# Performance work log

Measured on AMD Instinct MI355X. Metric: run time of the kernel, lower is better.

Reference implementation:

```python
import jax, jax.numpy as jnp
import numpy as np

N = 20000       # nodes
C = 64          # channels per irrep
E = 320000      # edges (avg degree 16)
S = 64          # num_species
R = 8           # radial embedding dim
HR = 64         # radial MLP hidden
HEADS = 2       # readout heads
AVG = 16.0      # avg_num_neighbors
SOFT = 2.0      # soft_normalization


def setup_inputs() -> dict:
    key = jax.random.key(0)
    ks = jax.random.split(key, 28)
    g = lambda k, sh, sc=1.0: jax.random.normal(k, sh, dtype=jnp.float32) * sc
    inv = lambda n: 1.0 / float(np.sqrt(n))
    return {
        "edge_vectors": g(ks[0], (E, 3)),
        "node_feats_s": g(ks[1], (N, C)),
        "node_feats_v": g(ks[2], (N, C, 3)),
        "radial_embeddings": g(ks[3], (E, R)),
        "node_species": jax.random.randint(ks[4], (N,), 0, S),
        "senders": jax.random.randint(ks[5], (E,), 0, N),
        "receivers": jax.random.randint(ks[6], (E,), 0, N),
        # residual FullyConnectedTensorProduct(feats, one-hot species) weights
        "W_rs": g(ks[7], (S, C, C), inv(C)),
        "W_rv": g(ks[8], (S, C, C), inv(C)),
        # interaction: linear up, radial MLP (5 TP paths), linear down
        "W_up_s": g(ks[9], (C, C), inv(C)),
        "W_up_v": g(ks[10], (C, C), inv(C)),
        "Wr1": g(ks[11], (R, HR), inv(R)),
        "Wr2": g(ks[12], (HR, 5 * C), inv(HR)),
        "W_down_s": g(ks[13], (C, C), inv(C)),
        "W_down_v": g(ks[14], (C, C), inv(C)),
        # equivariant product basis: per-channel species-indexed symmetric-contraction weights
        "w1s": g(ks[15], (S, C)),
        "w1v": g(ks[16], (S, C)),
        "w2ss": g(ks[17], (S, C)),
        "w2vv": g(ks[18], (S, C)),
        "w2sv": g(ks[19], (S, C)),
        "W_prod_s": g(ks[20], (C, C), inv(C)),
        "W_prod_v": g(ks[21], (C, C), inv(C)),
        # linear readout heads (out_irreps -> 1x0e per head)
        "w_read": g(ks[22], (HEADS, C), inv(C)),
    }


def reference(edge_vectors, node_feats_s, node_feats_v, radial_embeddings,
              node_species, senders, receivers,
              W_rs, W_rv, W_up_s, W_up_v, Wr1, Wr2, W_down_s, W_down_v,
              w1s, w1v, w2ss, w2vv, w2sv, W_prod_s, W_prod_v, w_read):
    n_nodes = node_feats_s.shape[0]
    sp = node_species

    # --- residual connection: FCTP(feats, one-hot(species)) == species-indexed channel mix
    res_s = jnp.einsum('nc,ncd->nd', node_feats_s, W_rs[sp])
    res_v = jnp.einsum('ncx,ncd->ndx', node_feats_v, W_rv[sp])

    # --- InteractionBlock ---
    s_u = node_feats_s @ W_up_s
    v_u = jnp.einsum('ncx,cd->ndx', node_feats_v, W_up_v)
    nrm = jnp.linalg.norm(edge_vectors, axis=-1, keepdims=True)
    u = edge_vectors / jnp.maximum(nrm, 1e-9)  # l=1 spherical harmonic direction [E,3]
    # radial MLP -> per-edge per-channel weights for the 5 CG paths of (0e+1o)x(0e+1o)->0e+1o
    w = (jax.nn.silu(radial_embeddings @ Wr1) @ Wr2).reshape(-1, 5, s_u.shape[1])
    se = s_u[senders]            # [E,C] gather (irregular)
    ve = v_u[senders]            # [E,C,3]
    dot = jnp.einsum('ecx,ex->ec', ve, u)          # 1o x 1o -> 0e
    crs = jnp.cross(ve, u[:, None, :])             # 1o x 1o -> 1o
    m_s = w[:, 0] * se + w[:, 3] * dot
    m_v = (w[:, 1][..., None] * ve
           + w[:, 2][..., None] * u[:, None, :]
           + w[:, 4][..., None] * crs)
    a_s = jax.ops.segment_sum(m_s, receivers, num_segments=n_nodes) / AVG
    a_v = jax.ops.segment_sum(m_v, receivers, num_segments=n_nodes) / AVG
    a_s = a_s @ W_down_s
    a_v = jnp.einsum('ncx,cd->ndx', a_v, W_down_v)

    # --- EquivariantProductBasisBlock: symmetric contraction (correlation<=2), per-channel
    # species-indexed weights, followed by a linear to out_irreps ---
    vv = jnp.sum(a_v * a_v, axis=-1)                                   # 1o (x) 1o -> 0e
    p_s = w1s[sp] * a_s + w2ss[sp] * a_s * a_s + w2vv[sp] * vv
    p_v = w1v[sp][..., None] * a_v + w2sv[sp][..., None] * a_s[..., None] * a_v
    p_s = p_s @ W_prod_s
    p_v = jnp.einsum('ncx,cd->ndx', p_v, W_prod_v)

    # --- soft normalization: phi(n) = 1/(1 + n*sus(n)), n = norm/SOFT ---
    def sus(x):
        return jnp.where(x > 0, jnp.exp(-1.0 / jnp.where(x > 0, x, 1.0)), 0.0)

    def phi(n):
        n = n / SOFT
        return 1.0 / (1.0 + n * sus(n))

    f_s = p_s * phi(jnp.abs(p_s))
    f_v = p_v * phi(jnp.linalg.norm(p_v, axis=-1, keepdims=True))

    # --- residual add ---
    f_s = f_s + res_s
    f_v = f_v + res_v

    # --- readout heads (Linear out_irreps -> 1x0e), stacked on axis=1 ---
    node_out = jnp.einsum('nc,hc->nh', f_s, w_read)
    return (node_out, f_s, f_v)
```

## Files before the change

kernel.cpp:

```cpp
#include <hip/hip_runtime.h>

#define N_NODES 20000
#define C 64
#define E_EDGES 320000
#define S_SPEC 64
#define R_DIM 8
#define HR 64
#define HEADS 2
#define TE 64
#define NT (E_EDGES/TE)
#define HPAD 68
#define INV_AVG (1.0f/16.0f)

#define FS_OFF 40000
#define FV_OFF 1320000

typedef short bf16x4 __attribute__((ext_vector_type(4)));
typedef float f32x4  __attribute__((ext_vector_type(4)));

__device__ __forceinline__ unsigned short f2bf(float f){
  unsigned u = __float_as_uint(f);
  u += 0x7fffu + ((u >> 16) & 1u);
  return (unsigned short)(u >> 16);
}
__device__ __forceinline__ float bf2f(unsigned short b){
  return __uint_as_float(((unsigned)b) << 16);
}
__device__ __forceinline__ float phi_f(float x){
  float n = x * 0.5f;
  float s = (n > 0.0f) ? expf(-1.0f/n) : 0.0f;
  return 1.0f / (1.0f + n * s);
}

__global__ __launch_bounds__(256) void wr2t_kernel(const float* __restrict__ Wr2,
                                                   unsigned short* __restrict__ wr2t){
  int idx = blockIdx.x*256 + threadIdx.x;
  int n = idx >> 6, k = idx & 63;
  wr2t[idx] = f2bf(Wr2[k*320 + n] * INV_AVG);
}

__global__ __launch_bounds__(256) void node_up_kernel(
    const float* __restrict__ fs, const float* __restrict__ fv,
    const float* __restrict__ Wus, const float* __restrict__ Wuv,
    ushort4* __restrict__ suv){
  const int ni = threadIdx.x >> 6;
  const int d  = threadIdx.x & 63;
  const int n  = blockIdx.x*4 + ni;
  __shared__ float s_l[4][C];
  __shared__ float v_l[4][3][C];
  s_l[ni][d] = fs[n*C + d];
  #pragma unroll
  for (int x = 0; x < 3; ++x) v_l[ni][x][d] = fv[(n*C + d)*3 + x];
  __syncthreads();
  float as = 0.f, a0 = 0.f, a1 = 0.f, a2 = 0.f;
  #pragma unroll 4
  for (int c = 0; c < C; ++c){
    float wsv = Wus[c*C + d];
    float wvv = Wuv[c*C + d];
    as += s_l[ni][c] * wsv;
    a0 += v_l[ni][0][c] * wvv;
    a1 += v_l[ni][1][c] * wvv;
    a2 += v_l[ni][2][c] * wvv;
  }
  ushort4 o;
  o.x = f2bf(as); o.y = f2bf(a0); o.z = f2bf(a1); o.w = f2bf(a2);
  suv[(size_t)n*C + d] = o;
}

__global__ __launch_bounds__(256) void hist_kernel(const int* __restrict__ rcv, int* __restrict__ count){
  int e = blockIdx.x*256 + threadIdx.x;
  atomicAdd(&count[rcv[e]], 1);
}

__global__ __launch_bounds__(1024) void scan_kernel(const int* __restrict__ count, int* __restrict__ cursor){
  __shared__ int sums[1024];
  const int t = threadIdx.x;
  const int base = t*20;
  int s = 0;
  #pragma unroll 4
  for (int i = 0; i < 20; ++i){ int idx = base+i; if (idx < N_NODES) s += count[idx]; }
  sums[t] = s;
  __syncthreads();
  for (int off = 1; off < 1024; off <<= 1){
    int v = (t >= off) ? sums[t-off] : 0;
    __syncthreads();
    sums[t] += v;
    __syncthreads();
  }
  int run = (t > 0) ? sums[t-1] : 0;
  for (int i = 0; i < 20; ++i){
    int idx = base+i;
    if (idx < N_NODES){ cursor[idx] = run; run += count[idx]; }
  }
}

__global__ __launch_bounds__(256) void scatter_kernel(
    const int* __restrict__ snd, const int* __restrict__ rcv,
    const float* __restrict__ ev, const float* __restrict__ re,
    int* __restrict__ cursor,
    int* __restrict__ snd_s, int* __restrict__ rcv_s,
    float4* __restrict__ u_s, float* __restrict__ re_s){
  int e = blockIdx.x*256 + threadIdx.x;
  int r = rcv[e];
  int pos = atomicAdd(&cursor[r], 1);
  snd_s[pos] = snd[e];
  rcv_s[pos] = r;
  float x = ev[e*3+0], y = ev[e*3+1], z = ev[e*3+2];
  float nr = sqrtf(x*x + y*y + z*z);
  float inv = 1.0f / fmaxf(nr, 1e-9f);
  float4 u4; u4.x = x*inv; u4.y = y*inv; u4.z = z*inv; u4.w = 0.f;
  u_s[pos] = u4;
  const float4* rp = (const float4*)&re[(size_t)e*R_DIM];
  float4 ra = rp[0], rb = rp[1];
  float4* op = (float4*)&re_s[(size_t)pos*R_DIM];
  op[0] = ra; op[1] = rb;
}

__global__ __launch_bounds__(512, 6) void edge_kernel(
    const float4* __restrict__ u_s, const float* __restrict__ re_s,
    const int* __restrict__ snd_s, const int* __restrict__ rcv_s,
    const float* __restrict__ Wr1, const unsigned short* __restrict__ wr2t,
    const ushort4* __restrict__ suv,
    float* __restrict__ a_s, float* __restrict__ a_v)
{
  __shared__ __align__(16) float Wr1_l[R_DIM*HR];
  __shared__ __align__(16) unsigned short Wr2T_l[320*HPAD];

  const int t = threadIdx.x;
  const int lane = t & 63;
  const int w = t >> 6;
  const int g  = w >> 1;
  const int h2 = w & 1;
  int b = blockIdx.x;
  int xcd = b & 7, idx = b >> 3;
  const int tile = xcd * (NT >> 3) + idx;
  const int e0 = tile * TE;

  Wr1_l[t] = Wr1[t];
  #pragma unroll
  for (int j = 0; j < 10; ++j){
    int i4 = t + 512*j;
    ushort4 v4 = ((const ushort4*)wr2t)[i4];
    int el = i4*4; int n = el >> 6, k = el & 63;
    *(ushort4*)&Wr2T_l[n*HPAD + k] = v4;
  }

  const int arow = g*16 + (lane & 15);
  const int koff = 4*(lane >> 4);
  const int cl = lane & 15;
  const int ebase = g*16 + (lane >> 4)*4;
  float4 ra = ((const float4*)&re_s[(size_t)(e0 + arow)*R_DIM])[0];
  float4 rb = ((const float4*)&re_s[(size_t)(e0 + arow)*R_DIM])[1];
  float u4x[4], u4y[4], u4z[4];
  int sn4[4], rc4[4];
  #pragma unroll
  for (int i = 0; i < 4; ++i){
    int e = e0 + ebase + i;
    float4 uu = u_s[e];
    u4x[i] = uu.x; u4y[i] = uu.y; u4z[i] = uu.z;
    sn4[i] = snd_s[e];
    rc4[i] = rcv_s[e];
  }
  __syncthreads();

  bf16x4 ha[4];
  #pragma unroll
  for (int kt = 0; kt < 4; ++kt){
    short4 tmp;
    #pragma unroll
    for (int j = 0; j < 4; ++j){
      int k = kt*16 + koff + j;
      float acc = ra.x*Wr1_l[0*HR+k] + ra.y*Wr1_l[1*HR+k] + ra.z*Wr1_l[2*HR+k] + ra.w*Wr1_l[3*HR+k]
                + rb.x*Wr1_l[4*HR+k] + rb.y*Wr1_l[5*HR+k] + rb.z*Wr1_l[6*HR+k] + rb.w*Wr1_l[7*HR+k];
      float sil = acc / (1.0f + expf(-acc));
      ((unsigned short*)&tmp)[j] = f2bf(sil);
    }
    ha[kt] = *(bf16x4*)&tmp;
  }

  ushort4 gv[4][2];
  #pragma unroll
  for (int i = 0; i < 4; ++i){
    const ushort4* sp_ = &suv[(size_t)sn4[i]*C];
    #pragma unroll
    for (int kk = 0; kk < 2; ++kk) gv[i][kk] = sp_[(2*h2 + kk)*16 + cl];
  }

  f32x4 acc[10];
  #pragma unroll
  for (int lf = 0; lf < 10; ++lf) acc[lf] = (f32x4){0.f,0.f,0.f,0.f};
  #pragma unroll
  for (int kt = 0; kt < 4; ++kt){
    bf16x4 af = ha[kt];
    #pragma unroll
    for (int lf = 0; lf < 10; ++lf){
      int p = lf >> 1, kk = lf & 1;
      int n = (p*4 + 2*h2 + kk)*16 + cl;
      bf16x4 bf = *(const bf16x4*)&Wr2T_l[n*HPAD + kt*16 + koff];
      acc[lf] = __builtin_amdgcn_mfma_f32_16x16x16bf16_1k(af, bf, acc[lf], 0, 0, 0);
    }
  }

  {
    float ms[2], mv0[2], mv1[2], mv2[2];
    #pragma unroll
    for (int kk = 0; kk < 2; ++kk){ ms[kk]=0.f; mv0[kk]=0.f; mv1[kk]=0.f; mv2[kk]=0.f; }
    int cur = rc4[0];
    #pragma unroll
    for (int i = 0; i < 4; ++i){
      int rc = rc4[i];
      if (rc != cur){
        #pragma unroll
        for (int kk = 0; kk < 2; ++kk){
          int c = (2*h2 + kk)*16 + cl;
          unsafeAtomicAdd(&a_s[cur*C + c],       ms[kk]);
          unsafeAtomicAdd(&a_v[(cur*3+0)*C + c], mv0[kk]);
          unsafeAtomicAdd(&a_v[(cur*3+1)*C + c], mv1[kk]);
          unsafeAtomicAdd(&a_v[(cur*3+2)*C + c], mv2[kk]);
          ms[kk]=0.f; mv0[kk]=0.f; mv1[kk]=0.f; mv2[kk]=0.f;
        }
        cur = rc;
      }
      float u0 = u4x[i], u1 = u4y[i], u2 = u4z[i];
      #pragma unroll
      for (int kk = 0; kk < 2; ++kk){
        float se  = bf2f(gv[i][kk].x);
        float ve0 = bf2f(gv[i][kk].y);
        float ve1 = bf2f(gv[i][kk].z);
        float ve2 = bf2f(gv[i][kk].w);
        float w0 = acc[0*2+kk][i];
        float w1 = acc[1*2+kk][i];
        float w2 = acc[2*2+kk][i];
        float w3 = acc[3*2+kk][i];
        float w4 = acc[4*2+kk][i];
        float dt  = ve0*u0 + ve1*u1 + ve2*u2;
        float cr0 = ve1*u2 - ve2*u1;
        float cr1 = ve2*u0 - ve0*u2;
        float cr2 = ve0*u1 - ve1*u0;
        ms[kk]  += w0*se + w3*dt;
        mv0[kk] += w1*ve0 + w2*u0 + w4*cr0;
        mv1[kk] += w1*ve1 + w2*u1 + w4*cr1;
        mv2[kk] += w1*ve2 + w2*u2 + w4*cr2;
      }
    }
    #pragma unroll
    for (int kk = 0; kk < 2; ++kk){
      int c = (2*h2 + kk)*16 + cl;
      unsafeAtomicAdd(&a_s[cur*C + c],       ms[kk]);
      unsafeAtomicAdd(&a_v[(cur*3+0)*C + c], mv0[kk]);
      unsafeAtomicAdd(&a_v[(cur*3+1)*C + c], mv1[kk]);
      unsafeAtomicAdd(&a_v[(cur*3+2)*C + c], mv2[kk]);
    }
  }
}

__global__ __launch_bounds__(256) void node_post_kernel(
    const float* __restrict__ a_s, const float* __restrict__ a_v,
    const float* __restrict__ fs_in, const float* __restrict__ fv_in,
    const int* __restrict__ species,
    const float* __restrict__ W_rs, const float* __restrict__ W_rv,
    const float* __restrict__ W_ds, const float* __restrict__ W_dv,
    const float* __restrict__ w1s, const float* __restrict__ w1v,
    const float* __restrict__ w2ss, const float* __restrict__ w2vv, const float* __restrict__ w2sv,
    const float* __restrict__ W_ps, const float* __restrict__ W_pv,
    const float* __restrict__ w_read, float* __restrict__ out)
{
  const int ni = threadIdx.x >> 6;
  const int d  = threadIdx.x & 63;
  const int n  = blockIdx.x*4 + ni;
  const int sp = species[n];
  __shared__ float as_l[4][C];
  __shared__ float av_l[4][3][C];
  __shared__ float si_l[4][C];
  __shared__ float vi_l[4][3][C];
  as_l[ni][d] = a_s[n*C + d];
  #pragma unroll
  for (int x=0;x<3;x++) av_l[ni][x][d] = a_v[(n*3+x)*C + d];
  si_l[ni][d] = fs_in[n*C + d];
  #pragma unroll
  for (int x=0;x<3;x++) vi_l[ni][x][d] = fv_in[(n*C + d)*3 + x];
  __syncthreads();
  const float* Wrs_p = W_rs + sp*C*C;
  const float* Wrv_p = W_rv + sp*C*C;
  float bs=0, bv0=0, bv1=0, bv2=0, rs=0, rv0=0, rv1=0, rv2=0;
  for (int c=0;c<C;++c){
    float wds = W_ds[c*C+d], wdv = W_dv[c*C+d];
    float wrs = Wrs_p[c*C+d], wrv = Wrv_p[c*C+d];
    bs  += as_l[ni][c]*wds;
    bv0 += av_l[ni][0][c]*wdv; bv1 += av_l[ni][1][c]*wdv; bv2 += av_l[ni][2][c]*wdv;
    rs  += si_l[ni][c]*wrs;
    rv0 += vi_l[ni][0][c]*wrv; rv1 += vi_l[ni][1][c]*wrv; rv2 += vi_l[ni][2][c]*wrv;
  }
  float vv = bv0*bv0 + bv1*bv1 + bv2*bv2;
  float ps  = w1s[sp*C+d]*bs + w2ss[sp*C+d]*bs*bs + w2vv[sp*C+d]*vv;
  float c1v = w1v[sp*C+d], c2sv = w2sv[sp*C+d];
  float pv0 = c1v*bv0 + c2sv*bs*bv0;
  float pv1 = c1v*bv1 + c2sv*bs*bv1;
  float pv2 = c1v*bv2 + c2sv*bs*bv2;
  __syncthreads();
  as_l[ni][d] = ps; av_l[ni][0][d]=pv0; av_l[ni][1][d]=pv1; av_l[ni][2][d]=pv2;
  __syncthreads();
  float qs=0, qv0=0, qv1=0, qv2=0;
  for (int c=0;c<C;++c){
    float wps = W_ps[c*C+d], wpv = W_pv[c*C+d];
    qs  += as_l[ni][c]*wps;
    qv0 += av_l[ni][0][c]*wpv; qv1 += av_l[ni][1][c]*wpv; qv2 += av_l[ni][2][c]*wpv;
  }
  float fsv = qs * phi_f(fabsf(qs)) + rs;
  float nv = sqrtf(qv0*qv0 + qv1*qv1 + qv2*qv2);
  float ph = phi_f(nv);
  float fv0 = qv0*ph + rv0;
  float fv1 = qv1*ph + rv1;
  float fv2 = qv2*ph + rv2;
  out[FS_OFF + n*C + d] = fsv;
  float* fvo = &out[FV_OFF + (size_t)(n*C + d)*3];
  fvo[0]=fv0; fvo[1]=fv1; fvo[2]=fv2;
  #pragma unroll
  for (int h=0; h<HEADS; ++h){
    float r = fsv * w_read[h*C + d];
    #pragma unroll
    for (int off=32; off>0; off>>=1) r += __shfl_down(r, off);
    if (d == 0) out[n*HEADS + h] = r;
  }
}

extern "C" void kernel_launch(void* const* d_in, const int* in_sizes, int n_in,
                              void* d_out, int out_size, void* d_ws, size_t ws_size,
                              hipStream_t stream)
{
  const float* ev   = (const float*)d_in[0];
  const float* nfs  = (const float*)d_in[1];
  const float* nfv  = (const float*)d_in[2];
  const float* re   = (const float*)d_in[3];
  const int*   spec = (const int*)d_in[4];
  const int*   snd  = (const int*)d_in[5];
  const int*   rcv  = (const int*)d_in[6];
  const float* W_rs = (const float*)d_in[7];
  const float* W_rv = (const float*)d_in[8];
  const float* Wus  = (const float*)d_in[9];
  const float* Wuv  = (const float*)d_in[10];
  const float* Wr1  = (const float*)d_in[11];
  const float* Wr2  = (const float*)d_in[12];
  const float* Wds  = (const float*)d_in[13];
  const float* Wdv  = (const float*)d_in[14];
  const float* w1s  = (const float*)d_in[15];
  const float* w1v  = (const float*)d_in[16];
  const float* w2ss = (const float*)d_in[17];
  const float* w2vv = (const float*)d_in[18];
  const float* w2sv = (const float*)d_in[19];
  const float* Wps  = (const float*)d_in[20];
  const float* Wpv  = (const float*)d_in[21];
  const float* wrd  = (const float*)d_in[22];

  float* out = (float*)d_out;
  float* ws  = (float*)d_ws;
  ushort4* suv  = (ushort4*)ws;
  float*   a_s  = ws + 2560000;
  float*   a_v  = ws + 3840000;
  int*    count = (int*)(ws + 7680000);
  int*    cursr = (int*)(ws + 7700000);
  int*    snd_s = (int*)(ws + 7720000);
  int*    rcv_s = (int*)(ws + 8040000);
  float4* u_s   = (float4*)(ws + 8360000);
  float*  re_s  = ws + 9640000;
  unsigned short* wr2t = (unsigned short*)(ws + 12200000);

  hipMemsetAsync(a_s, 0, (size_t)5120000*sizeof(float), stream);
  hipMemsetAsync(count, 0, (size_t)N_NODES*sizeof(int), stream);

  wr2t_kernel<<<(320*64)/256, 256, 0, stream>>>(Wr2, wr2t);
  node_up_kernel<<<N_NODES/4, 256, 0, stream>>>(nfs, nfv, Wus, Wuv, suv);
  hist_kernel<<<E_EDGES/256, 256, 0, stream>>>(rcv, count);
  scan_kernel<<<1, 1024, 0, stream>>>(count, cursr);
  scatter_kernel<<<E_EDGES/256, 256, 0, stream>>>(snd, rcv, ev, re, cursr,
                                                  snd_s, rcv_s, u_s, re_s);
  edge_kernel<<<NT, 512, 0, stream>>>(u_s, re_s, snd_s, rcv_s, Wr1, wr2t,
                                      suv, a_s, a_v);
  node_post_kernel<<<N_NODES/4, 256, 0, stream>>>(a_s, a_v, nfs, nfv, spec,
      W_rs, W_rv, Wds, Wdv, w1s, w1v, w2ss, w2vv, w2sv, Wps, Wpv, wrd, out);
}
```

Before: 409.1 us.

## Move node GEMMs to bf16 MFMA and group residual GEMM by species

The per-node scalar dot-product kernels are replaced by 64-node tiles computed with bf16 16x16x16 MFMA instructions. This covers the up-projection, the down-projection and the product linear. The species-indexed residual tensor product is split into its own GEMM kernel over a species-sorted node permutation, built by new histogram, scan and permute kernels. Each block then loads one species' weight matrix once, instead of every node fetching its own 64x64 slice. The residual is stored as bf16 in the workspace that the up-projection used, which adds bf16 rounding to residual and post-node results and adds several small launches.

```diff
diff --git a/kernel.cpp b/kernel.cpp
--- a/kernel.cpp
+++ b/kernel.cpp
@@ -11,6 +11,8 @@
 #define NT (E_EDGES/TE)
 #define HPAD 68
 #define INV_AVG (1.0f/16.0f)
+#define NB 64
+#define NNB ((N_NODES + NB - 1)/NB)
 
 #define FS_OFF 40000
 #define FV_OFF 1320000
@@ -39,32 +41,78 @@
   wr2t[idx] = f2bf(Wr2[k*320 + n] * INV_AVG);
 }
 
-__global__ __launch_bounds__(256) void node_up_kernel(
+__global__ __launch_bounds__(256) void node_up_mfma(
     const float* __restrict__ fs, const float* __restrict__ fv,
     const float* __restrict__ Wus, const float* __restrict__ Wuv,
     ushort4* __restrict__ suv){
-  const int ni = threadIdx.x >> 6;
-  const int d  = threadIdx.x & 63;
-  const int n  = blockIdx.x*4 + ni;
-  __shared__ float s_l[4][C];
-  __shared__ float v_l[4][3][C];
-  s_l[ni][d] = fs[n*C + d];
-  #pragma unroll
-  for (int x = 0; x < 3; ++x) v_l[ni][x][d] = fv[(n*C + d)*3 + x];
+  __shared__ __align__(16) unsigned short A[4][NB][HPAD];
+  __shared__ __align__(16) unsigned short B[2][NB][HPAD];
+  const int t = threadIdx.x;
+  const int n0 = blockIdx.x * NB;
+  #pragma unroll
+  for (int j = 0; j < 4; ++j){
+    int el = (t + 256*j)*4; int row = el >> 6, c = el & 63;
+    float4 v = (n0+row < N_NODES) ? *(const float4*)&fs[(size_t)(n0+row)*C + c]
+                                  : (float4){0,0,0,0};
+    ushort4 o; o.x=f2bf(v.x); o.y=f2bf(v.y); o.z=f2bf(v.z); o.w=f2bf(v.w);
+    *(ushort4*)&A[0][row][c] = o;
+  }
+  #pragma unroll
+  for (int j = 0; j < 16; ++j){
+    int el = t + 256*j; int row = el >> 6, c = el & 63;
+    float x=0,y=0,z=0;
+    if (n0+row < N_NODES){
+      const float* p = &fv[((size_t)(n0+row)*C + c)*3];
+      x = p[0]; y = p[1]; z = p[2];
+    }
+    A[1][row][c] = f2bf(x); A[2][row][c] = f2bf(y); A[3][row][c] = f2bf(z);
+  }
+  #pragma unroll
+  for (int j = 0; j < 16; ++j){
+    int el = t + 256*j; int c = el >> 6, d = el & 63;
+    B[0][d][c] = f2bf(Wus[c*C + d]);
+    B[1][d][c] = f2bf(Wuv[c*C + d]);
+  }
   __syncthreads();
-  float as = 0.f, a0 = 0.f, a1 = 0.f, a2 = 0.f;
-  #pragma unroll 4
-  for (int c = 0; c < C; ++c){
-    float wsv = Wus[c*C + d];
-    float wvv = Wuv[c*C + d];
-    as += s_l[ni][c] * wsv;
-    a0 += v_l[ni][0][c] * wvv;
-    a1 += v_l[ni][1][c] * wvv;
-    a2 += v_l[ni][2][c] * wvv;
-  }
-  ushort4 o;
-  o.x = f2bf(as); o.y = f2bf(a0); o.z = f2bf(a1); o.w = f2bf(a2);
-  suv[(size_t)n*C + d] = o;
+  const int lane = t & 63, w = t >> 6;
+  const int arow = w*16 + (lane & 15);
+  const int koff = 4*(lane >> 4);
+  f32x4 acc[4][4];
+  #pragma unroll
+  for (int a=0;a<4;a++)
+    #pragma unroll
+    for (int cf=0;cf<4;cf++) acc[a][cf] = (f32x4){0,0,0,0};
+  #pragma unroll
+  for (int kt = 0; kt < 4; ++kt){
+    bf16x4 a0 = *(const bf16x4*)&A[0][arow][kt*16+koff];
+    bf16x4 a1 = *(const bf16x4*)&A[1][arow][kt*16+koff];
+    bf16x4 a2 = *(const bf16x4*)&A[2][arow][kt*16+koff];
+    bf16x4 a3 = *(const bf16x4*)&A[3][arow][kt*16+koff];
+    #pragma unroll
+    for (int cf = 0; cf < 4; ++cf){
+      const int brow = cf*16 + (lane & 15);
+      bf16x4 b0 = *(const bf16x4*)&B[0][brow][kt*16+koff];
+      bf16x4 b1 = *(const bf16x4*)&B[1][brow][kt*16+koff];
+      acc[0][cf] = __builtin_amdgcn_mfma_f32_16x16x16bf16_1k(a0, b0, acc[0][cf], 0,0,0);
+      acc[1][cf] = __builtin_amdgcn_mfma_f32_16x16x16bf16_1k(a1, b1, acc[1][cf], 0,0,0);
+      acc[2][cf] = __builtin_amdgcn_mfma_f32_16x16x16bf16_1k(a2, b1, acc[2][cf], 0,0,0);
+      acc[3][cf] = __builtin_amdgcn_mfma_f32_16x16x16bf16_1k(a3, b1, acc[3][cf], 0,0,0);
+    }
+  }
+  #pragma unroll
+  for (int i = 0; i < 4; ++i){
+    int n = n0 + w*16 + (lane>>4)*4 + i;
+    if (n < N_NODES){
+      #pragma unroll
+      for (int cf = 0; cf < 4; ++cf){
+        int c = cf*16 + (lane & 15);
+        ushort4 o;
+        o.x = f2bf(acc[0][cf][i]); o.y = f2bf(acc[1][cf][i]);
+        o.z = f2bf(acc[2][cf][i]); o.w = f2bf(acc[3][cf][i]);
+        suv[(size_t)n*C + c] = o;
+      }
+    }
+  }
 }
 
 __global__ __launch_bounds__(256) void hist_kernel(const int* __restrict__ rcv, int* __restrict__ count){
@@ -114,6 +162,109 @@
   float4 ra = rp[0], rb = rp[1];
   float4* op = (float4*)&re_s[(size_t)pos*R_DIM];
   op[0] = ra; op[1] = rb;
+}
+
+__global__ __launch_bounds__(256) void sp_hist_kernel(const int* __restrict__ sp, int* __restrict__ spcount){
+  int n = blockIdx.x*256 + threadIdx.x;
+  if (n < N_NODES) atomicAdd(&spcount[sp[n]], 1);
+}
+__global__ __launch_bounds__(64) void sp_scan_kernel(const int* __restrict__ spcount,
+                                                     int* __restrict__ spoff, int* __restrict__ spcur){
+  if (threadIdx.x == 0){
+    int run = 0;
+    for (int i = 0; i < S_SPEC; ++i){ spoff[i] = run; spcur[i] = run; run += spcount[i]; }
+    spoff[S_SPEC] = run;
+  }
+}
+__global__ __launch_bounds__(256) void sp_perm_kernel(const int* __restrict__ sp,
+                                                      int* __restrict__ spcur, int* __restrict__ perm_sp){
+  int n = blockIdx.x*256 + threadIdx.x;
+  if (n < N_NODES){
+    int pos = atomicAdd(&spcur[sp[n]], 1);
+    perm_sp[pos] = n;
+  }
+}
+
+__global__ __launch_bounds__(256) void residual_gemm(
+    const float* __restrict__ nfs, const float* __restrict__ nfv,
+    const float* __restrict__ W_rs, const float* __restrict__ W_rv,
+    const int* __restrict__ spoff, const int* __restrict__ perm_sp,
+    ushort4* __restrict__ resp){
+  const int s = blockIdx.x >> 3;
+  const int chunk = blockIdx.x & 7;
+  const int base = spoff[s];
+  const int cnt  = spoff[s+1] - base;
+  const int r0 = chunk * NB;
+  if (r0 >= cnt) return;
+  const int rows = min(NB, cnt - r0);
+  __shared__ __align__(16) unsigned short A[4][NB][HPAD];
+  __shared__ __align__(16) unsigned short B[2][NB][HPAD];
+  __shared__ int nid[NB];
+  const int t = threadIdx.x;
+  if (t < NB) nid[t] = (t < rows) ? perm_sp[base + r0 + t] : -1;
+  __syncthreads();
+  #pragma unroll
+  for (int j = 0; j < 16; ++j){
+    int el = t + 256*j; int row = el >> 6, c = el & 63;
+    int n = nid[row];
+    float sv=0, x=0, y=0, z=0;
+    if (n >= 0){
+      sv = nfs[(size_t)n*C + c];
+      const float* p = &nfv[((size_t)n*C + c)*3];
+      x = p[0]; y = p[1]; z = p[2];
+    }
+    A[0][row][c] = f2bf(sv); A[1][row][c] = f2bf(x);
+    A[2][row][c] = f2bf(y);  A[3][row][c] = f2bf(z);
+  }
+  const float* Ws = W_rs + (size_t)s*C*C;
+  const float* Wv = W_rv + (size_t)s*C*C;
+  #pragma unroll
+  for (int j = 0; j < 16; ++j){
+    int el = t + 256*j; int c = el >> 6, d = el & 63;
+    B[0][d][c] = f2bf(Ws[c*C + d]);
+    B[1][d][c] = f2bf(Wv[c*C + d]);
+  }
+  __syncthreads();
+  const int lane = t & 63, w = t >> 6;
+  const int arow = w*16 + (lane & 15);
+  const int koff = 4*(lane >> 4);
+  f32x4 acc[4][4];
+  #pragma unroll
+  for (int a=0;a<4;a++)
+    #pragma unroll
+    for (int cf=0;cf<4;cf++) acc[a][cf] = (f32x4){0,0,0,0};
+  #pragma unroll
+  for (int kt = 0; kt < 4; ++kt){
+    bf16x4 a0 = *(const bf16x4*)&A[0][arow][kt*16+koff];
+    bf16x4 a1 = *(const bf16x4*)&A[1][arow][kt*16+koff];
+    bf16x4 a2 = *(const bf16x4*)&A[2][arow][kt*16+koff];
+    bf16x4 a3 = *(const bf16x4*)&A[3][arow][kt*16+koff];
+    #pragma unroll
+    for (int cf = 0; cf < 4; ++cf){
+      const int brow = cf*16 + (lane & 15);
+      bf16x4 b0 = *(const bf16x4*)&B[0][brow][kt*16+koff];
+      bf16x4 b1 = *(const bf16x4*)&B[1][brow][kt*16+koff];
+      acc[0][cf] = __builtin_amdgcn_mfma_f32_16x16x16bf16_1k(a0, b0, acc[0][cf], 0,0,0);
+      acc[1][cf] = __builtin_amdgcn_mfma_f32_16x16x16bf16_1k(a1, b1, acc[1][cf], 0,0,0);
+      acc[2][cf] = __builtin_amdgcn_mfma_f32_16x16x16bf16_1k(a2, b1, acc[2][cf], 0,0,0);
+      acc[3][cf] = __builtin_amdgcn_mfma_f32_16x16x16bf16_1k(a3, b1, acc[3][cf], 0,0,0);
+    }
+  }
+  #pragma unroll
+  for (int i = 0; i < 4; ++i){
+    int row = w*16 + (lane>>4)*4 + i;
+    int n = nid[row];
+    if (n >= 0){
+      #pragma unroll
+      for (int cf = 0; cf < 4; ++cf){
+        int c = cf*16 + (lane & 15);
+        ushort4 o;
+        o.x = f2bf(acc[0][cf][i]); o.y = f2bf(acc[1][cf][i]);
+        o.z = f2bf(acc[2][cf][i]); o.w = f2bf(acc[3][cf][i]);
+        resp[(size_t)n*C + c] = o;
+      }
+    }
+  }
 }
 
 __global__ __launch_bounds__(512, 6) void edge_kernel(
@@ -254,73 +405,158 @@
   }
 }
 
-__global__ __launch_bounds__(256) void node_post_kernel(
+__global__ __launch_bounds__(256) void node_post_mfma(
     const float* __restrict__ a_s, const float* __restrict__ a_v,
-    const float* __restrict__ fs_in, const float* __restrict__ fv_in,
     const int* __restrict__ species,
-    const float* __restrict__ W_rs, const float* __restrict__ W_rv,
     const float* __restrict__ W_ds, const float* __restrict__ W_dv,
     const float* __restrict__ w1s, const float* __restrict__ w1v,
     const float* __restrict__ w2ss, const float* __restrict__ w2vv, const float* __restrict__ w2sv,
     const float* __restrict__ W_ps, const float* __restrict__ W_pv,
+    const ushort4* __restrict__ resp,
     const float* __restrict__ w_read, float* __restrict__ out)
 {
-  const int ni = threadIdx.x >> 6;
-  const int d  = threadIdx.x & 63;
-  const int n  = blockIdx.x*4 + ni;
-  const int sp = species[n];
-  __shared__ float as_l[4][C];
-  __shared__ float av_l[4][3][C];
-  __shared__ float si_l[4][C];
-  __shared__ float vi_l[4][3][C];
-  as_l[ni][d] = a_s[n*C + d];
-  #pragma unroll
-  for (int x=0;x<3;x++) av_l[ni][x][d] = a_v[(n*3+x)*C + d];
-  si_l[ni][d] = fs_in[n*C + d];
-  #pragma unroll
-  for (int x=0;x<3;x++) vi_l[ni][x][d] = fv_in[(n*C + d)*3 + x];
+  __shared__ __align__(16) unsigned short A[4][NB][HPAD];
+  __shared__ __align__(16) unsigned short B[4][NB][HPAD];
+  __shared__ int spl[NB];
+  const int t = threadIdx.x;
+  const int n0 = blockIdx.x * NB;
+  #pragma unroll
+  for (int j = 0; j < 4; ++j){
+    int el = (t + 256*j)*4; int row = el >> 6, c = el & 63;
+    bool ok = (n0+row < N_NODES);
+    float4 v0 = ok ? *(const float4*)&a_s[(size_t)(n0+row)*C + c] : (float4){0,0,0,0};
+    ushort4 o0; o0.x=f2bf(v0.x); o0.y=f2bf(v0.y); o0.z=f2bf(v0.z); o0.w=f2bf(v0.w);
+    *(ushort4*)&A[0][row][c] = o0;
+    #pragma unroll
+    for (int x = 0; x < 3; ++x){
+      float4 v = ok ? *(const float4*)&a_v[((size_t)(n0+row)*3 + x)*C + c] : (float4){0,0,0,0};
+      ushort4 o; o.x=f2bf(v.x); o.y=f2bf(v.y); o.z=f2bf(v.z); o.w=f2bf(v.w);
+      *(ushort4*)&A[1+x][row][c] = o;
+    }
+  }
+  #pragma unroll
+  for (int j = 0; j < 16; ++j){
+    int el = t + 256*j; int c = el >> 6, d = el & 63;
+    B[0][d][c] = f2bf(W_ds[c*C + d]);
+    B[1][d][c] = f2bf(W_dv[c*C + d]);
+    B[2][d][c] = f2bf(W_ps[c*C + d]);
+    B[3][d][c] = f2bf(W_pv[c*C + d]);
+  }
+  if (t < NB) spl[t] = (n0 + t < N_NODES) ? species[n0 + t] : 0;
   __syncthreads();
-  const float* Wrs_p = W_rs + sp*C*C;
-  const float* Wrv_p = W_rv + sp*C*C;
-  float bs=0, bv0=0, bv1=0, bv2=0, rs=0, rv0=0, rv1=0, rv2=0;
-  for (int c=0;c<C;++c){
-    float wds = W_ds[c*C+d], wdv = W_dv[c*C+d];
-    float wrs = Wrs_p[c*C+d], wrv = Wrv_p[c*C+d];
-    bs  += as_l[ni][c]*wds;
-    bv0 += av_l[ni][0][c]*wdv; bv1 += av_l[ni][1][c]*wdv; bv2 += av_l[ni][2][c]*wdv;
-    rs  += si_l[ni][c]*wrs;
-    rv0 += vi_l[ni][0][c]*wrv; rv1 += vi_l[ni][1][c]*wrv; rv2 += vi_l[ni][2][c]*wrv;
-  }
-  float vv = bv0*bv0 + bv1*bv1 + bv2*bv2;
-  float ps  = w1s[sp*C+d]*bs + w2ss[sp*C+d]*bs*bs + w2vv[sp*C+d]*vv;
-  float c1v = w1v[sp*C+d], c2sv = w2sv[sp*C+d];
-  float pv0 = c1v*bv0 + c2sv*bs*bv0;
-  float pv1 = c1v*bv1 + c2sv*bs*bv1;
-  float pv2 = c1v*bv2 + c2sv*bs*bv2;
+
+  const int lane = t & 63, w = t >> 6;
+  const int arow = w*16 + (lane & 15);
+  const int koff = 4*(lane >> 4);
+  const int cl = lane & 15;
+
+  f32x4 acc1[4][4];
+  #pragma unroll
+  for (int a=0;a<4;a++)
+    #pragma unroll
+    for (int cf=0;cf<4;cf++) acc1[a][cf] = (f32x4){0,0,0,0};
+  #pragma unroll
+  for (int kt = 0; kt < 4; ++kt){
+    bf16x4 a0 = *(const bf16x4*)&A[0][arow][kt*16+koff];
+    bf16x4 a1 = *(const bf16x4*)&A[1][arow][kt*16+koff];
+    bf16x4 a2 = *(const bf16x4*)&A[2][arow][kt*16+koff];
+    bf16x4 a3 = *(const bf16x4*)&A[3][arow][kt*16+koff];
+    #pragma unroll
+    for (int cf = 0; cf < 4; ++cf){
+      const int brow = cf*16 + (lane & 15);
+      bf16x4 b0 = *(const bf16x4*)&B[0][brow][kt*16+koff];
+      bf16x4 b1 = *(const bf16x4*)&B[1][brow][kt*16+koff];
+      acc1[0][cf] = __builtin_amdgcn_mfma_f32_16x16x16bf16_1k(a0, b0, acc1[0][cf], 0,0,0);
+      acc1[1][cf] = __builtin_amdgcn_mfma_f32_16x16x16bf16_1k(a1, b1, acc1[1][cf], 0,0,0);
+      acc1[2][cf] = __builtin_amdgcn_mfma_f32_16x16x16bf16_1k(a2, b1, acc1[2][cf], 0,0,0);
+      acc1[3][cf] = __builtin_amdgcn_mfma_f32_16x16x16bf16_1k(a3, b1, acc1[3][cf], 0,0,0);
+    }
+  }
+  #pragma unroll
+  for (int i = 0; i < 4; ++i){
+    int row = w*16 + (lane>>4)*4 + i;
+    int sp = spl[row];
+    #pragma unroll
+    for (int cf = 0; cf < 4; ++cf){
+      int c = cf*16 + cl;
+      float bs = acc1[0][cf][i], bv0 = acc1[1][cf][i], bv1 = acc1[2][cf][i], bv2 = acc1[3][cf][i];
+      float vv = bv0*bv0 + bv1*bv1 + bv2*bv2;
+      float ps = w1s[sp*C+c]*bs + w2ss[sp*C+c]*bs*bs + w2vv[sp*C+c]*vv;
+      float c1v = w1v[sp*C+c], c2sv = w2sv[sp*C+c];
+      A[0][row][c] = f2bf(ps);
+      A[1][row][c] = f2bf(c1v*bv0 + c2sv*bs*bv0);
+      A[2][row][c] = f2bf(c1v*bv1 + c2sv*bs*bv1);
+      A[3][row][c] = f2bf(c1v*bv2 + c2sv*bs*bv2);
+    }
+  }
   __syncthreads();
-  as_l[ni][d] = ps; av_l[ni][0][d]=pv0; av_l[ni][1][d]=pv1; av_l[ni][2][d]=pv2;
-  __syncthreads();
-  float qs=0, qv0=0, qv1=0, qv2=0;
-  for (int c=0;c<C;++c){
-    float wps = W_ps[c*C+d], wpv = W_pv[c*C+d];
-    qs  += as_l[ni][c]*wps;
-    qv0 += av_l[ni][0][c]*wpv; qv1 += av_l[ni][1][c]*wpv; qv2 += av_l[ni][2][c]*wpv;
-  }
-  float fsv = qs * phi_f(fabsf(qs)) + rs;
-  float nv = sqrtf(qv0*qv0 + qv1*qv1 + qv2*qv2);
-  float ph = phi_f(nv);
-  float fv0 = qv0*ph + rv0;
-  float fv1 = qv1*ph + rv1;
-  float fv2 = qv2*ph + rv2;
-  out[FS_OFF + n*C + d] = fsv;
-  float* fvo = &out[FV_OFF + (size_t)(n*C + d)*3];
-  fvo[0]=fv0; fvo[1]=fv1; fvo[2]=fv2;
-  #pragma unroll
-  for (int h=0; h<HEADS; ++h){
-    float r = fsv * w_read[h*C + d];
-    #pragma unroll
-    for (int off=32; off>0; off>>=1) r += __shfl_down(r, off);
-    if (d == 0) out[n*HEADS + h] = r;
+  f32x4 acc2[4][4];
+  #pragma unroll
+  for (int a=0;a<4;a++)
+    #pragma unroll
+    for (int cf=0;cf<4;cf++) acc2[a][cf] = (f32x4){0,0,0,0};
+  #pragma unroll
+  for (int kt = 0; kt < 4; ++kt){
+    bf16x4 a0 = *(const bf16x4*)&A[0][arow][kt*16+koff];
+    bf16x4 a1 = *(const bf16x4*)&A[1][arow][kt*16+koff];
+    bf16x4 a2 = *(const bf16x4*)&A[2][arow][kt*16+koff];
+    bf16x4 a3 = *(const bf16x4*)&A[3][arow][kt*16+koff];
+    #pragma unroll
+    for (int cf = 0; cf < 4; ++cf){
+      const int brow = cf*16 + (lane & 15);
+      bf16x4 b2 = *(const bf16x4*)&B[2][brow][kt*16+koff];
+      bf16x4 b3 = *(const bf16x4*)&B[3][brow][kt*16+koff];
+      acc2[0][cf] = __builtin_amdgcn_mfma_f32_16x16x16bf16_1k(a0, b2, acc2[0][cf], 0,0,0);
+      acc2[1][cf] = __builtin_amdgcn_mfma_f32_16x16x16bf16_1k(a1, b3, acc2[1][cf], 0,0,0);
+      acc2[2][cf] = __builtin_amdgcn_mfma_f32_16x16x16bf16_1k(a2, b3, acc2[2][cf], 0,0,0);
+      acc2[3][cf] = __builtin_amdgcn_mfma_f32_16x16x16bf16_1k(a3, b3, acc2[3][cf], 0,0,0);
+    }
+  }
+  float fsv_r[4][4];
+  #pragma unroll
+  for (int i = 0; i < 4; ++i){
+    int row = w*16 + (lane>>4)*4 + i;
+    int n = n0 + row;
+    bool ok = (n < N_NODES);
+    #pragma unroll
+    for (int cf = 0; cf < 4; ++cf){
+      int c = cf*16 + cl;
+      float qs = acc2[0][cf][i], qv0 = acc2[1][cf][i], qv1 = acc2[2][cf][i], qv2 = acc2[3][cf][i];
+      float rs = 0, rv0 = 0, rv1 = 0, rv2 = 0;
+      if (ok){
+        ushort4 rp = resp[(size_t)n*C + c];
+        rs  = bf2f(rp.x); rv0 = bf2f(rp.y); rv1 = bf2f(rp.z); rv2 = bf2f(rp.w);
+      }
+      float fsv = qs * phi_f(fabsf(qs)) + rs;
+      float nv = sqrtf(qv0*qv0 + qv1*qv1 + qv2*qv2);
+      float ph = phi_f(nv);
+      float fv0 = qv0*ph + rv0;
+      float fv1 = qv1*ph + rv1;
+      float fv2 = qv2*ph + rv2;
+      fsv_r[i][cf] = fsv;
+      if (ok){
+        out[FS_OFF + (size_t)n*C + c] = fsv;
+        float* fvo = &out[FV_OFF + ((size_t)n*C + c)*3];
+        fvo[0] = fv0; fvo[1] = fv1; fvo[2] = fv2;
+      }
+    }
+  }
+  #pragma unroll
+  for (int h = 0; h < HEADS; ++h){
+    #pragma unroll
+    for (int i = 0; i < 4; ++i){
+      int row = w*16 + (lane>>4)*4 + i;
+      int n = n0 + row;
+      float tacc = 0.f;
+      #pragma unroll
+      for (int cf = 0; cf < 4; ++cf)
+        tacc += fsv_r[i][cf] * w_read[h*C + cf*16 + cl];
+      tacc += __shfl_xor(tacc, 1);
+      tacc += __shfl_xor(tacc, 2);
+      tacc += __shfl_xor(tacc, 4);
+      tacc += __shfl_xor(tacc, 8);
+      if (cl == 0 && n < N_NODES) out[(size_t)n*HEADS + h] = tacc;
+    }
   }
 }
 
@@ -355,6 +591,7 @@
   float* out = (float*)d_out;
   float* ws  = (float*)d_ws;
   ushort4* suv  = (ushort4*)ws;
+  ushort4* resp = (ushort4*)ws;
   float*   a_s  = ws + 2560000;
   float*   a_v  = ws + 3840000;
   int*    count = (int*)(ws + 7680000);
@@ -364,18 +601,28 @@
   float4* u_s   = (float4*)(ws + 8360000);
   float*  re_s  = ws + 9640000;
   unsigned short* wr2t = (unsigned short*)(ws + 12200000);
+  int*   spcount= (int*)(ws + 12210240);
+  int*   spoff  = (int*)(ws + 12210304);
+  int*   spcur  = (int*)(ws + 12210432);
+  int*   perm_sp= (int*)(ws + 12210496);
 
   hipMemsetAsync(a_s, 0, (size_t)5120000*sizeof(float), stream);
   hipMemsetAsync(count, 0, (size_t)N_NODES*sizeof(int), stream);
+  hipMemsetAsync(spcount, 0, (size_t)S_SPEC*sizeof(int), stream);
 
   wr2t_kernel<<<(320*64)/256, 256, 0, stream>>>(Wr2, wr2t);
-  node_up_kernel<<<N_NODES/4, 256, 0, stream>>>(nfs, nfv, Wus, Wuv, suv);
+  node_up_mfma<<<NNB, 256, 0, stream>>>(nfs, nfv, Wus, Wuv, suv);
   hist_kernel<<<E_EDGES/256, 256, 0, stream>>>(rcv, count);
   scan_kernel<<<1, 1024, 0, stream>>>(count, cursr);
   scatter_kernel<<<E_EDGES/256, 256, 0, stream>>>(snd, rcv, ev, re, cursr,
                                                   snd_s, rcv_s, u_s, re_s);
+  sp_hist_kernel<<<(N_NODES+255)/256, 256, 0, stream>>>(spec, spcount);
+  sp_scan_kernel<<<1, 64, 0, stream>>>(spcount, spoff, spcur);
+  sp_perm_kernel<<<(N_NODES+255)/256, 256, 0, stream>>>(spec, spcur, perm_sp);
   edge_kernel<<<NT, 512, 0, stream>>>(u_s, re_s, snd_s, rcv_s, Wr1, wr2t,
                                       suv, a_s, a_v);
-  node_post_kernel<<<N_NODES/4, 256, 0, stream>>>(a_s, a_v, nfs, nfv, spec,
-      W_rs, W_rv, Wds, Wdv, w1s, w1v, w2ss, w2vv, w2sv, Wps, Wpv, wrd, out);
-}
+  residual_gemm<<<S_SPEC*8, 256, 0, stream>>>(nfs, nfv, W_rs, W_rv, spoff, perm_sp,
+                                              resp);
+  node_post_mfma<<<NNB, 256, 0, stream>>>(a_s, a_v, spec, Wds, Wdv,
+      w1s, w1v, w2ss, w2vv, w2sv, Wps, Wpv, resp, wrd, out);
+}
```

Result: slower. 434.4 us (+6.2%).

## Process two edge tiles per block with software-pipelined loads

Applied to the files above, without the earlier changes.

Each edge-kernel block now handles two 64-edge tiles instead of one. The Wr2 weight staging into LDS is paid once for both tiles, and loads for the second tile (edge data, sender gathers) are issued while the first tile's MFMA and accumulation run. Launch bounds drop from 6 to 4 blocks per CU to leave room for the extra live registers, and the XCD tile mapping is generalised for a non-multiple-of-8 count. The cost is lower occupancy and more register pressure.

```diff
diff --git a/kernel.cpp b/kernel.cpp
--- a/kernel.cpp
+++ b/kernel.cpp
@@ -8,7 +8,7 @@
 #define HR 64
 #define HEADS 2
 #define TE 64
-#define NT (E_EDGES/TE)
+#define NPAIR (E_EDGES/128)
 #define HPAD 68
 #define INV_AVG (1.0f/16.0f)
 
@@ -116,7 +116,7 @@
   op[0] = ra; op[1] = rb;
 }
 
-__global__ __launch_bounds__(512, 6) void edge_kernel(
+__global__ __launch_bounds__(512, 4) void edge_kernel(
     const float4* __restrict__ u_s, const float* __restrict__ re_s,
     const int* __restrict__ snd_s, const int* __restrict__ rcv_s,
     const float* __restrict__ Wr1, const unsigned short* __restrict__ wr2t,
@@ -133,8 +133,10 @@
   const int h2 = w & 1;
   int b = blockIdx.x;
   int xcd = b & 7, idx = b >> 3;
-  const int tile = xcd * (NT >> 3) + idx;
-  const int e0 = tile * TE;
+  const int q = NPAIR >> 3, r = NPAIR & 7;
+  int pair = (xcd < r ? xcd*(q+1) : r*(q+1) + (xcd-r)*q) + idx;
+  const int e0A = pair * 128;
+  const int e0B = e0A + 64;
 
   Wr1_l[t] = Wr1[t];
   #pragma unroll
@@ -149,66 +151,83 @@
   const int koff = 4*(lane >> 4);
   const int cl = lane & 15;
   const int ebase = g*16 + (lane >> 4)*4;
-  float4 ra = ((const float4*)&re_s[(size_t)(e0 + arow)*R_DIM])[0];
-  float4 rb = ((const float4*)&re_s[(size_t)(e0 + arow)*R_DIM])[1];
-  float u4x[4], u4y[4], u4z[4];
-  int sn4[4], rc4[4];
+
+  float4 raA = ((const float4*)&re_s[(size_t)(e0A + arow)*R_DIM])[0];
+  float4 rbA = ((const float4*)&re_s[(size_t)(e0A + arow)*R_DIM])[1];
+  float uxA[4], uyA[4], uzA[4]; int snA[4], rcA[4];
   #pragma unroll
   for (int i = 0; i < 4; ++i){
-    int e = e0 + ebase + i;
+    int e = e0A + ebase + i;
     float4 uu = u_s[e];
-    u4x[i] = uu.x; u4y[i] = uu.y; u4z[i] = uu.z;
-    sn4[i] = snd_s[e];
-    rc4[i] = rcv_s[e];
-  }
-  __syncthreads();
-
-  bf16x4 ha[4];
+    uxA[i]=uu.x; uyA[i]=uu.y; uzA[i]=uu.z;
+    snA[i]=snd_s[e]; rcA[i]=rcv_s[e];
+  }
+  ushort4 gvA[4][2];
+  #pragma unroll
+  for (int i = 0; i < 4; ++i){
+    const ushort4* sp_ = &suv[(size_t)snA[i]*C];
+    #pragma unroll
+    for (int kk = 0; kk < 2; ++kk) gvA[i][kk] = sp_[(2*h2 + kk)*16 + cl];
+  }
+  __syncthreads();
+
+  bf16x4 haA[4];
   #pragma unroll
   for (int kt = 0; kt < 4; ++kt){
     short4 tmp;
     #pragma unroll
     for (int j = 0; j < 4; ++j){
       int k = kt*16 + koff + j;
-      float acc = ra.x*Wr1_l[0*HR+k] + ra.y*Wr1_l[1*HR+k] + ra.z*Wr1_l[2*HR+k] + ra.w*Wr1_l[3*HR+k]
-                + rb.x*Wr1_l[4*HR+k] + rb.y*Wr1_l[5*HR+k] + rb.z*Wr1_l[6*HR+k] + rb.w*Wr1_l[7*HR+k];
+      float acc = raA.x*Wr1_l[0*HR+k] + raA.y*Wr1_l[1*HR+k] + raA.z*Wr1_l[2*HR+k] + raA.w*Wr1_l[3*HR+k]
+                + rbA.x*Wr1_l[4*HR+k] + rbA.y*Wr1_l[5*HR+k] + rbA.z*Wr1_l[6*HR+k] + rbA.w*Wr1_l[7*HR+k];
       float sil = acc / (1.0f + expf(-acc));
       ((unsigned short*)&tmp)[j] = f2bf(sil);
     }
-    ha[kt] = *(bf16x4*)&tmp;
-  }
-
-  ushort4 gv[4][2];
+    haA[kt] = *(bf16x4*)&tmp;
+  }
+
+  float4 raB = ((const float4*)&re_s[(size_t)(e0B + arow)*R_DIM])[0];
+  float4 rbB = ((const float4*)&re_s[(size_t)(e0B + arow)*R_DIM])[1];
+  float uxB[4], uyB[4], uzB[4]; int snB[4], rcB[4];
   #pragma unroll
   for (int i = 0; i < 4; ++i){
-    const ushort4* sp_ = &suv[(size_t)sn4[i]*C];
-    #pragma unroll
-    for (int kk = 0; kk < 2; ++kk) gv[i][kk] = sp_[(2*h2 + kk)*16 + cl];
-  }
-
-  f32x4 acc[10];
-  #pragma unroll
-  for (int lf = 0; lf < 10; ++lf) acc[lf] = (f32x4){0.f,0.f,0.f,0.f};
+    int e = e0B + ebase + i;
+    float4 uu = u_s[e];
+    uxB[i]=uu.x; uyB[i]=uu.y; uzB[i]=uu.z;
+    snB[i]=snd_s[e]; rcB[i]=rcv_s[e];
+  }
+
+  f32x4 accA[10];
+  #pragma unroll
+  for (int lf = 0; lf < 10; ++lf) accA[lf] = (f32x4){0.f,0.f,0.f,0.f};
   #pragma unroll
   for (int kt = 0; kt < 4; ++kt){
-    bf16x4 af = ha[kt];
+    bf16x4 af = haA[kt];
     #pragma unroll
     for (int lf = 0; lf < 10; ++lf){
       int p = lf >> 1, kk = lf & 1;
       int n = (p*4 + 2*h2 + kk)*16 + cl;
       bf16x4 bf = *(const bf16x4*)&Wr2T_l[n*HPAD + kt*16 + koff];
-      acc[lf] = __builtin_amdgcn_mfma_f32_16x16x16bf16_1k(af, bf, acc[lf], 0, 0, 0);
-    }
+      accA[lf] = __builtin_amdgcn_mfma_f32_16x16x16bf16_1k(af, bf, accA[lf], 0, 0, 0);
+    }
+  }
+
+  ushort4 gvB[4][2];
+  #pragma unroll
+  for (int i = 0; i < 4; ++i){
+    const ushort4* sp_ = &suv[(size_t)snB[i]*C];
+    #pragma unroll
+    for (int kk = 0; kk < 2; ++kk) gvB[i][kk] = sp_[(2*h2 + kk)*16 + cl];
   }
 
   {
     float ms[2], mv0[2], mv1[2], mv2[2];
     #pragma unroll
     for (int kk = 0; kk < 2; ++kk){ ms[kk]=0.f; mv0[kk]=0.f; mv1[kk]=0.f; mv2[kk]=0.f; }
-    int cur = rc4[0];
+    int cur = rcA[0];
     #pragma unroll
     for (int i = 0; i < 4; ++i){
-      int rc = rc4[i];
+      int rc = rcA[i];
       if (rc != cur){
         #pragma unroll
         for (int kk = 0; kk < 2; ++kk){
@@ -221,18 +240,99 @@
         }
         cur = rc;
       }
-      float u0 = u4x[i], u1 = u4y[i], u2 = u4z[i];
+      float u0 = uxA[i], u1 = uyA[i], u2 = uzA[i];
       #pragma unroll
       for (int kk = 0; kk < 2; ++kk){
-        float se  = bf2f(gv[i][kk].x);
-        float ve0 = bf2f(gv[i][kk].y);
-        float ve1 = bf2f(gv[i][kk].z);
-        float ve2 = bf2f(gv[i][kk].w);
-        float w0 = acc[0*2+kk][i];
-        float w1 = acc[1*2+kk][i];
-        float w2 = acc[2*2+kk][i];
-        float w3 = acc[3*2+kk][i];
-        float w4 = acc[4*2+kk][i];
+        float se  = bf2f(gvA[i][kk].x);
+        float ve0 = bf2f(gvA[i][kk].y);
+        float ve1 = bf2f(gvA[i][kk].z);
+        float ve2 = bf2f(gvA[i][kk].w);
+        float w0 = accA[0*2+kk][i];
+        float w1 = accA[1*2+kk][i];
+        float w2 = accA[2*2+kk][i];
+        float w3 = accA[3*2+kk][i];
+        float w4 = accA[4*2+kk][i];
+        float dt  = ve0*u0 + ve1*u1 + ve2*u2;
+        float cr0 = ve1*u2 - ve2*u1;
+        float cr1 = ve2*u0 - ve0*u2;
+        float cr2 = ve0*u1 - ve1*u0;
+        ms[kk]  += w0*se + w3*dt;
+        mv0[kk] += w1*ve0 + w2*u0 + w4*cr0;
+        mv1[kk] += w1*ve1 + w2*u1 + w4*cr1;
+        mv2[kk] += w1*ve2 + w2*u2 + w4*cr2;
+      }
+    }
+    #pragma unroll
+    for (int kk = 0; kk < 2; ++kk){
+      int c = (2*h2 + kk)*16 + cl;
+      unsafeAtomicAdd(&a_s[cur*C + c],       ms[kk]);
+      unsafeAtomicAdd(&a_v[(cur*3+0)*C + c], mv0[kk]);
+      unsafeAtomicAdd(&a_v[(cur*3+1)*C + c], mv1[kk]);
+      unsafeAtomicAdd(&a_v[(cur*3+2)*C + c], mv2[kk]);
+    }
+  }
+
+  bf16x4 haB[4];
+  #pragma unroll
+  for (int kt = 0; kt < 4; ++kt){
+    short4 tmp;
+    #pragma unroll
+    for (int j = 0; j < 4; ++j){
+      int k = kt*16 + koff + j;
+      float acc = raB.x*Wr1_l[0*HR+k] + raB.y*Wr1_l[1*HR+k] + raB.z*Wr1_l[2*HR+k] + raB.w*Wr1_l[3*HR+k]
+                + rbB.x*Wr1_l[4*HR+k] + rbB.y*Wr1_l[5*HR+k] + rbB.z*Wr1_l[6*HR+k] + rbB.w*Wr1_l[7*HR+k];
+      float sil = acc / (1.0f + expf(-acc));
+      ((unsigned short*)&tmp)[j] = f2bf(sil);
+    }
+    haB[kt] = *(bf16x4*)&tmp;
+  }
+  f32x4 accB[10];
+  #pragma unroll
+  for (int lf = 0; lf < 10; ++lf) accB[lf] = (f32x4){0.f,0.f,0.f,0.f};
+  #pragma unroll
+  for (int kt = 0; kt < 4; ++kt){
+    bf16x4 af = haB[kt];
+    #pragma unroll
+    for (int lf = 0; lf < 10; ++lf){
+      int p = lf >> 1, kk = lf & 1;
+      int n = (p*4 + 2*h2 + kk)*16 + cl;
+      bf16x4 bf = *(const bf16x4*)&Wr2T_l[n*HPAD + kt*16 + koff];
+      accB[lf] = __builtin_amdgcn_mfma_f32_16x16x16bf16_1k(af, bf, accB[lf], 0, 0, 0);
+    }
+  }
+
+  {
+    float ms[2], mv0[2], mv1[2], mv2[2];
+    #pragma unroll
+    for (int kk = 0; kk < 2; ++kk){ ms[kk]=0.f; mv0[kk]=0.f; mv1[kk]=0.f; mv2[kk]=0.f; }
+    int cur = rcB[0];
+    #pragma unroll
+    for (int i = 0; i < 4; ++i){
+      int rc = rcB[i];
+      if (rc != cur){
+        #pragma unroll
+        for (int kk = 0; kk < 2; ++kk){
+          int c = (2*h2 + kk)*16 + cl;
+          unsafeAtomicAdd(&a_s[cur*C + c],       ms[kk]);
+          unsafeAtomicAdd(&a_v[(cur*3+0)*C + c], mv0[kk]);
+          unsafeAtomicAdd(&a_v[(cur*3+1)*C + c], mv1[kk]);
+          unsafeAtomicAdd(&a_v[(cur*3+2)*C + c], mv2[kk]);
+          ms[kk]=0.f; mv0[kk]=0.f; mv1[kk]=0.f; mv2[kk]=0.f;
+        }
+        cur = rc;
+      }
+      float u0 = uxB[i], u1 = uyB[i], u2 = uzB[i];
+      #pragma unroll
+      for (int kk = 0; kk < 2; ++kk){
+        float se  = bf2f(gvB[i][kk].x);
+        float ve0 = bf2f(gvB[i][kk].y);
+        float ve1 = bf2f(gvB[i][kk].z);
+        float ve2 = bf2f(gvB[i][kk].w);
+        float w0 = accB[0*2+kk][i];
+        float w1 = accB[1*2+kk][i];
+        float w2 = accB[2*2+kk][i];
+        float w3 = accB[3*2+kk][i];
+        float w4 = accB[4*2+kk][i];
         float dt  = ve0*u0 + ve1*u1 + ve2*u2;
         float cr0 = ve1*u2 - ve2*u1;
         float cr1 = ve2*u0 - ve0*u2;
@@ -374,8 +474,8 @@
   scan_kernel<<<1, 1024, 0, stream>>>(count, cursr);
   scatter_kernel<<<E_EDGES/256, 256, 0, stream>>>(snd, rcv, ev, re, cursr,
                                                   snd_s, rcv_s, u_s, re_s);
-  edge_kernel<<<NT, 512, 0, stream>>>(u_s, re_s, snd_s, rcv_s, Wr1, wr2t,
-                                      suv, a_s, a_v);
+  edge_kernel<<<NPAIR, 512, 0, stream>>>(u_s, re_s, snd_s, rcv_s, Wr1, wr2t,
+                                         suv, a_s, a_v);
   node_post_kernel<<<N_NODES/4, 256, 0, stream>>>(a_s, a_v, nfs, nfv, spec,
       W_rs, W_rv, Wds, Wdv, w1s, w1v, w2ss, w2vv, w2sv, Wps, Wpv, wrd, out);
 }
```

Measured after the change: 399.8 us. -2.3%, faster.
